# Performance work log

Measured on AMD Instinct MI355X. Metric: run time of the kernel, lower is better.

## Reference

```python
import jax, jax.numpy as jnp
import numpy as np

N_NODES = 100000


def _gcn_norm(edge_index, num_nodes):
    # PyG GCNConv default: add self-loops, symmetric normalization.
    src = jnp.concatenate([edge_index[0], jnp.arange(num_nodes, dtype=edge_index.dtype)])
    dst = jnp.concatenate([edge_index[1], jnp.arange(num_nodes, dtype=edge_index.dtype)])
    deg = jax.ops.segment_sum(jnp.ones_like(dst, dtype=jnp.float32), dst, num_segments=num_nodes)
    dis = jnp.where(deg > 0, jax.lax.rsqrt(deg), 0.0)  # deg^{-1/2}
    norm = dis[src] * dis[dst]  # [E + N]
    return src, dst, norm


def _gcn_conv(x, W, b, src, dst, norm, num_nodes):
    h = x @ W.T                      # [N, out] transform first (out < in)
    msg = h[src] * norm[:, None]     # gather + per-edge scale
    agg = jax.ops.segment_sum(msg, dst, num_segments=num_nodes)  # scatter-add
    return agg + b


def setup_inputs() -> dict:
    key = jax.random.key(0)
    ks = jax.random.split(key, 12)
    E = 3200000
    x = jax.random.normal(ks[0], (N_NODES, 128), dtype=jnp.float32)
    edge_index = jax.random.randint(ks[1], (2, E), 0, N_NODES, dtype=jnp.int64)
    s = lambda k, sh, fan: jax.random.normal(k, sh, dtype=jnp.float32) * (1.0 / np.sqrt(fan))
    return {
        "x": x,
        "edge_index": edge_index,
        "W1": s(ks[2], (32, 128), 128), "b1": jnp.zeros((32,), jnp.float32),
        "W2": s(ks[3], (16, 32), 32),   "b2": jnp.zeros((16,), jnp.float32),
        "w_ih": s(ks[4], (32, 16), 16), "w_hh": s(ks[5], (32, 8), 8),
        "b_ih": s(ks[6], (32,), 8),     "b_hh": s(ks[7], (32,), 8),
        "W_out": s(ks[8], (1, 8), 8),   "b_out": jnp.zeros((1,), jnp.float32),
    }


def reference(x, edge_index, W1, b1, W2, b2, w_ih, w_hh, b_ih, b_hh, W_out, b_out):
    src, dst, norm = _gcn_norm(edge_index, N_NODES)
    h = jax.nn.relu(_gcn_conv(x, W1, b1, src, dst, norm, N_NODES))   # [N, 32]
    h = jax.nn.relu(_gcn_conv(h, W2, b2, src, dst, norm, N_NODES))   # [N, 16]
    # Single-timestep LSTM with h0 = c0 = 0 (gate order: i, f, g, o).
    gates = h @ w_ih.T + b_ih + b_hh   # [N, 32]; h0 @ w_hh.T term is zero
    i, f, g, o = jnp.split(gates, 4, axis=-1)
    c = jax.nn.sigmoid(i) * jnp.tanh(g)
    hh = jax.nn.sigmoid(o) * jnp.tanh(c)  # [N, 8]
    out = hh @ W_out.T + b_out            # [N, 1]
    return out.squeeze(-1)                # [N]
```

## Files before the change

kernel.cpp:

```cpp
#include <hip/hip_runtime.h>
#include <hip/hip_fp16.h>
#include <math.h>

static constexpr int N = 100000;
static constexpr int SHIFT = 7;
static constexpr int BUCKN = 1 << SHIFT;
static constexpr int NBUCK = (N + BUCKN - 1) >> SHIFT;
static constexpr int CHUNK = 16384;
static constexpr int STRIDE = 5120;
static constexpr int COLCAP = NBUCK * STRIDE;

__global__ __launch_bounds__(1024) void k_init(int* __restrict__ gcur) {
    int b = threadIdx.x;
    if (b < NBUCK) gcur[b] = b * STRIDE;
}

__global__ __launch_bounds__(1024) void k_part(const int* __restrict__ src,
                                               const int* __restrict__ dst,
                                               int* __restrict__ gcur,
                                               int* __restrict__ col, int E) {
    __shared__ int hl[NBUCK];
    __shared__ int cur[NBUCK];
    const int t = threadIdx.x, b = blockIdx.x;
    if (t < NBUCK) hl[t] = 0;
    __syncthreads();
    const int e0 = b * CHUNK;
    const int m = min(CHUNK, E - e0);
    for (int i = t; i < m; i += 1024) atomicAdd(&hl[dst[e0 + i] >> SHIFT], 1);
    __syncthreads();
    if (t < NBUCK) cur[t] = atomicAdd(&gcur[t], hl[t]);
    __syncthreads();
    for (int i = t; i < m; i += 1024) {
        int d = dst[e0 + i];
        int pos = atomicAdd(&cur[d >> SHIFT], 1);
        pos = min(max(pos, 0), COLCAP - 1);
        col[pos] = (src[e0 + i] & 0x1FFFF) | ((d & (BUCKN - 1)) << 17);
    }
}

__global__ __launch_bounds__(1024) void k_sort(const int* __restrict__ gcur,
                                               int* __restrict__ col,
                                               int* __restrict__ deg,
                                               int* __restrict__ row_start) {
    __shared__ int es[STRIDE];
    __shared__ int cnt[BUCKN];
    __shared__ int cur[BUCKN];
    const int t = threadIdx.x, buck = blockIdx.x;
    const int s0 = buck * STRIDE;
    int n = gcur[buck] - s0;
    n = max(0, min(n, STRIDE));
    if (t < BUCKN) cnt[t] = 0;
    __syncthreads();
    for (int i = t; i < n; i += 1024) {
        int p = col[s0 + i];
        es[i] = p;
        atomicAdd(&cnt[(p >> 17) & (BUCKN - 1)], 1);
    }
    __syncthreads();
    if (t < BUCKN) cur[t] = cnt[t];
    __syncthreads();
    for (int off = 1; off < BUCKN; off <<= 1) {
        int v = (t < BUCKN && t >= off) ? cur[t - off] : 0;
        __syncthreads();
        if (t < BUCKN) cur[t] += v;
        __syncthreads();
    }
    if (t < BUCKN) {
        int excl = cur[t] - cnt[t];
        int node = buck * BUCKN + t;
        if (node < N) {
            deg[node] = cnt[t];
            row_start[node] = s0 + excl;
        }
        cur[t] = excl;
    }
    __syncthreads();
    for (int i = t; i < n; i += 1024) {
        int p = es[i];
        int pos = atomicAdd(&cur[(p >> 17) & (BUCKN - 1)], 1);
        pos = min(max(pos, 0), STRIDE - 1);
        col[s0 + pos] = p & 0x1FFFF;
    }
}

__global__ __launch_bounds__(256) void k_xw1(
        const float* __restrict__ x, const float* __restrict__ W1,
        const int* __restrict__ deg, __half* __restrict__ g1h) {
    __shared__ float4 wtv[32 * 33];
    __shared__ float4 xsv[1024];
    const int t = threadIdx.x;
    const float4* W1v = (const float4*)W1;
    for (int idx = t; idx < 1024; idx += 256) {
        int j = idx >> 5, kb = idx & 31;
        wtv[kb * 33 + j] = W1v[idx];
    }
    const float4* x4 = (const float4*)x + (size_t)blockIdx.x * 1024;
    for (int idx = t; idx < 1024; idx += 256) xsv[idx] = x4[idx];
    __syncthreads();

    const int j = t & 31, ng = t >> 5;
    float a0 = 0.f, a1 = 0.f, a2 = 0.f, a3 = 0.f;
#pragma unroll 4
    for (int kb = 0; kb < 32; ++kb) {
        float4 w = wtv[kb * 33 + j];
        float4 x0 = xsv[(4 * ng + 0) * 32 + kb];
        float4 x1 = xsv[(4 * ng + 1) * 32 + kb];
        float4 x2 = xsv[(4 * ng + 2) * 32 + kb];
        float4 x3 = xsv[(4 * ng + 3) * 32 + kb];
        a0 = fmaf(w.x, x0.x, fmaf(w.y, x0.y, fmaf(w.z, x0.z, fmaf(w.w, x0.w, a0))));
        a1 = fmaf(w.x, x1.x, fmaf(w.y, x1.y, fmaf(w.z, x1.z, fmaf(w.w, x1.w, a1))));
        a2 = fmaf(w.x, x2.x, fmaf(w.y, x2.y, fmaf(w.z, x2.z, fmaf(w.w, x2.w, a2))));
        a3 = fmaf(w.x, x3.x, fmaf(w.y, x3.y, fmaf(w.z, x3.z, fmaf(w.w, x3.w, a3))));
    }
    const int nb = blockIdx.x * 32 + 4 * ng;
    g1h[(nb + 0) * 32 + j] = __float2half(a0 * rsqrtf((float)(deg[nb + 0] + 1)));
    g1h[(nb + 1) * 32 + j] = __float2half(a1 * rsqrtf((float)(deg[nb + 1] + 1)));
    g1h[(nb + 2) * 32 + j] = __float2half(a2 * rsqrtf((float)(deg[nb + 2] + 1)));
    g1h[(nb + 3) * 32 + j] = __float2half(a3 * rsqrtf((float)(deg[nb + 3] + 1)));
}

__global__ __launch_bounds__(256) void k_gather1(
        const int* __restrict__ row_start, const int* __restrict__ deg,
        const int* __restrict__ col, const __half* __restrict__ g1h,
        const float* __restrict__ b1, const float* __restrict__ W2,
        __half* __restrict__ g2h) {
    __shared__ float h1s[64 * 33];
    __shared__ float w2t[32 * 17];
    const int t = threadIdx.x;
    for (int idx = t; idx < 512; idx += 256) {
        int j = idx >> 5, k = idx & 31;
        w2t[k * 17 + j] = W2[idx];
    }
    const int lane = t & 63, w = t >> 6;
    const int q = lane & 3;
    const int nloc = w * 16 + (lane >> 2);
    const int node = blockIdx.x * 64 + nloc;
    const int nc = node < N ? node : N - 1;
    const int rs = row_start[nc];
    const int ne = (node < N) ? deg[nc] : 0;
    const uint4* g1v = (const uint4*)g1h;

    float acc[8];
    {
        uint4 rv = g1v[nc * 4 + q];
        const __half2* hp = (const __half2*)&rv;
#pragma unroll
        for (int m2 = 0; m2 < 4; ++m2) {
            float2 f = __half22float2(hp[m2]);
            acc[2 * m2] = f.x;
            acc[2 * m2 + 1] = f.y;
        }
    }
    for (int base = 0; base < ne; base += 16) {
        int sv[4];
#pragma unroll
        for (int c = 0; c < 4; ++c)
            sv[c] = (base + 4 * c + q < ne) ? col[rs + base + 4 * c + q] : 0;
        int idx[16];
#pragma unroll
        for (int c = 0; c < 4; ++c)
#pragma unroll
            for (int u = 0; u < 4; ++u)
                idx[4 * c + u] = min(__shfl(sv[c], u, 4), N - 1);
        uint4 rv[16];
#pragma unroll
        for (int u = 0; u < 16; ++u) rv[u] = g1v[idx[u] * 4 + q];
#pragma unroll
        for (int u = 0; u < 16; ++u) {
            float wt = (base + u < ne) ? 1.f : 0.f;
            const __half2* hp = (const __half2*)&rv[u];
#pragma unroll
            for (int m2 = 0; m2 < 4; ++m2) {
                float2 f = __half22float2(hp[m2]);
                acc[2 * m2]     = fmaf(wt, f.x, acc[2 * m2]);
                acc[2 * m2 + 1] = fmaf(wt, f.y, acc[2 * m2 + 1]);
            }
        }
    }
    {
        const float dis = rsqrtf((float)(ne + 1));
#pragma unroll
        for (int u = 0; u < 8; ++u) {
            float v = (node < N) ? (acc[u] * dis + b1[q * 8 + u]) : 0.f;
            h1s[nloc * 33 + q * 8 + u] = v > 0.f ? v : 0.f;
        }
    }
    __syncthreads();
    const int n2 = t >> 2, jq = (t & 3) * 4;
    const int node2 = blockIdx.x * 64 + n2;
    if (node2 < N) {
        float a0 = 0.f, a1 = 0.f, a2 = 0.f, a3 = 0.f;
        const float* hr = h1s + n2 * 33;
#pragma unroll
        for (int k = 0; k < 32; ++k) {
            float h = hr[k];
            a0 = fmaf(h, w2t[k * 17 + jq + 0], a0);
            a1 = fmaf(h, w2t[k * 17 + jq + 1], a1);
            a2 = fmaf(h, w2t[k * 17 + jq + 2], a2);
            a3 = fmaf(h, w2t[k * 17 + jq + 3], a3);
        }
        const float dis2 = rsqrtf((float)(deg[node2] + 1));
        __half2* g2p = (__half2*)(g2h + node2 * 16 + jq);
        g2p[0] = __floats2half2_rn(a0 * dis2, a1 * dis2);
        g2p[1] = __floats2half2_rn(a2 * dis2, a3 * dis2);
    }
}

__global__ __launch_bounds__(256) void k_gather2(
        const int* __restrict__ row_start, const int* __restrict__ deg,
        const int* __restrict__ col, const __half* __restrict__ g2h,
        const float* __restrict__ b2, float* __restrict__ h2) {
    const int t = threadIdx.x;
    const int lane = t & 63, w = t >> 6;
    const int q = lane & 1;
    const int node = blockIdx.x * 128 + w * 32 + (lane >> 1);
    const int nc = node < N ? node : N - 1;
    const int rs = row_start[nc];
    const int ne = (node < N) ? deg[nc] : 0;
    const uint4* g2v = (const uint4*)g2h;

    float acc[8];
    {
        uint4 rv = g2v[nc * 2 + q];
        const __half2* hp = (const __half2*)&rv;
#pragma unroll
        for (int m2 = 0; m2 < 4; ++m2) {
            float2 f = __half22float2(hp[m2]);
            acc[2 * m2] = f.x;
            acc[2 * m2 + 1] = f.y;
        }
    }
    for (int base = 0; base < ne; base += 16) {
        int sv[8];
#pragma unroll
        for (int c = 0; c < 8; ++c)
            sv[c] = (base + 2 * c + q < ne) ? col[rs + base + 2 * c + q] : 0;
        int idx[16];
#pragma unroll
        for (int c = 0; c < 8; ++c) {
            idx[2 * c]     = min(__shfl(sv[c], 0, 2), N - 1);
            idx[2 * c + 1] = min(__shfl(sv[c], 1, 2), N - 1);
        }
        uint4 rv[16];
#pragma unroll
        for (int u = 0; u < 16; ++u) rv[u] = g2v[idx[u] * 2 + q];
#pragma unroll
        for (int u = 0; u < 16; ++u) {
            float wt = (base + u < ne) ? 1.f : 0.f;
            const __half2* hp = (const __half2*)&rv[u];
#pragma unroll
            for (int m2 = 0; m2 < 4; ++m2) {
                float2 f = __half22float2(hp[m2]);
                acc[2 * m2]     = fmaf(wt, f.x, acc[2 * m2]);
                acc[2 * m2 + 1] = fmaf(wt, f.y, acc[2 * m2 + 1]);
            }
        }
    }
    if (node < N) {
        const float dis = rsqrtf((float)(ne + 1));
        float4* h2v = (float4*)h2;
#pragma unroll
        for (int h = 0; h < 2; ++h) {
            float4 o;
            float v0 = acc[4 * h + 0] * dis + b2[q * 8 + 4 * h + 0];
            float v1 = acc[4 * h + 1] * dis + b2[q * 8 + 4 * h + 1];
            float v2 = acc[4 * h + 2] * dis + b2[q * 8 + 4 * h + 2];
            float v3 = acc[4 * h + 3] * dis + b2[q * 8 + 4 * h + 3];
            o.x = v0 > 0.f ? v0 : 0.f;
            o.y = v1 > 0.f ? v1 : 0.f;
            o.z = v2 > 0.f ? v2 : 0.f;
            o.w = v3 > 0.f ? v3 : 0.f;
            h2v[node * 4 + q * 2 + h] = o;
        }
    }
}

__global__ __launch_bounds__(256) void k_final(
        const float* __restrict__ h2g,
        const float* __restrict__ w_ih, const float* __restrict__ b_ih,
        const float* __restrict__ b_hh, const float* __restrict__ W_out,
        const float* __restrict__ b_out, float* __restrict__ out) {
    __shared__ float wih[512];
    __shared__ float bias[32];
    __shared__ float wout[8];
    __shared__ float bo;
    const int t = threadIdx.x;
    for (int idx = t; idx < 512; idx += 256) wih[idx] = w_ih[idx];
    if (t < 32) bias[t] = b_ih[t] + b_hh[t];
    if (t < 8)  wout[t] = W_out[t];
    if (t == 0) bo = b_out[0];
    __syncthreads();

    const int i = blockIdx.x * 256 + t;
    if (i >= N) return;
    float h2[16];
    const float4* a4 = (const float4*)(h2g + (size_t)i * 16);
#pragma unroll
    for (int q = 0; q < 4; ++q) {
        float4 v = a4[q];
        h2[q * 4 + 0] = v.x; h2[q * 4 + 1] = v.y;
        h2[q * 4 + 2] = v.z; h2[q * 4 + 3] = v.w;
    }
    float oacc = 0.f;
#pragma unroll
    for (int q = 0; q < 8; ++q) {
        float gi = bias[q], gg = bias[16 + q], go = bias[24 + q];
#pragma unroll
        for (int k = 0; k < 16; ++k) {
            gi = fmaf(h2[k], wih[q * 16 + k], gi);
            gg = fmaf(h2[k], wih[(16 + q) * 16 + k], gg);
            go = fmaf(h2[k], wih[(24 + q) * 16 + k], go);
        }
        float c  = (1.f / (1.f + expf(-gi))) * tanhf(gg);
        float hh = (1.f / (1.f + expf(-go))) * tanhf(c);
        oacc = fmaf(hh, wout[q], oacc);
    }
    out[i] = oacc + bo;
}

extern "C" void kernel_launch(void* const* d_in, const int* in_sizes, int n_in,
                              void* d_out, int out_size, void* d_ws, size_t ws_size,
                              hipStream_t stream) {
    const float* x     = (const float*)d_in[0];
    const int*   ei    = (const int*)d_in[1];
    const float* W1    = (const float*)d_in[2];
    const float* b1    = (const float*)d_in[3];
    const float* W2    = (const float*)d_in[4];
    const float* b2    = (const float*)d_in[5];
    const float* w_ih  = (const float*)d_in[6];
    const float* b_ih  = (const float*)d_in[8];
    const float* b_hh  = (const float*)d_in[9];
    const float* W_out = (const float*)d_in[10];
    const float* b_out = (const float*)d_in[11];
    float* out = (float*)d_out;

    const int E = in_sizes[1] / 2;
    const int* src = ei;
    const int* dst = ei + E;
    const int BP = (E + CHUNK - 1) / CHUNK;

    int* col       = (int*)d_ws;
    int* deg       = col + COLCAP;
    int* row_start = deg + N;
    int* gcur      = row_start + N;
    int* base2     = gcur + 784;
    __half* g1h    = (__half*)base2;
    __half* g2h    = (__half*)(base2 + (size_t)N * 16);
    float* h2      = (float*)(base2 + (size_t)N * 24);

    k_init   <<<1,               1024, 0, stream>>>(gcur);
    k_part   <<<BP,              1024, 0, stream>>>(src, dst, gcur, col, E);
    k_sort   <<<NBUCK,           1024, 0, stream>>>(gcur, col, deg, row_start);
    k_xw1    <<<N / 32,          256,  0, stream>>>(x, W1, deg, g1h);
    k_gather1<<<(N + 63) / 64,   256,  0, stream>>>(row_start, deg, col, g1h, b1, W2, g2h);
    k_gather2<<<(N + 127) / 128, 256,  0, stream>>>(row_start, deg, col, g2h, b2, h2);
    k_final  <<<(N + 255) / 256, 256,  0, stream>>>(h2, w_ih, b_ih, b_hh, W_out, b_out, out);
}
```

Measured before the change: 257.9 us.

## Replace global-atomic bucket partition with block-local sorted chunks and header-driven gather

The partition kernel now sorts each chunk by bucket in shared memory and writes it out contiguously with per-block bucket offsets in a header table, instead of scattering edges through global atomic cursors. The sort kernel then gathers its bucket's runs from every chunk using a prefix sum over the headers, and writes the CSR columns into a separate array. The goal is coalesced writes, no global atomics and no init kernel. In exchange, the sort kernel reads many short, serially-walked runs per bucket, one thread per source chunk with a per-element loop, which may be slow.

Measured after the change: 261.7 us. No clear change (+1.5%).

```diff
diff --git a/kernel.cpp b/kernel.cpp
--- a/kernel.cpp
+++ b/kernel.cpp
@@ -6,21 +6,21 @@
 static constexpr int SHIFT = 7;
 static constexpr int BUCKN = 1 << SHIFT;
 static constexpr int NBUCK = (N + BUCKN - 1) >> SHIFT;
-static constexpr int CHUNK = 16384;
+static constexpr int HDRS  = NBUCK + 1;
+static constexpr int CHUNK = 8192;
+static constexpr int BPMAX = 512;
 static constexpr int STRIDE = 5120;
 static constexpr int COLCAP = NBUCK * STRIDE;
-
-__global__ __launch_bounds__(1024) void k_init(int* __restrict__ gcur) {
-    int b = threadIdx.x;
-    if (b < NBUCK) gcur[b] = b * STRIDE;
-}
+static constexpr int ES_CAP = STRIDE;
 
 __global__ __launch_bounds__(1024) void k_part(const int* __restrict__ src,
                                                const int* __restrict__ dst,
-                                               int* __restrict__ gcur,
-                                               int* __restrict__ col, int E) {
+                                               int* __restrict__ col,
+                                               int* __restrict__ hdr, int E) {
+    __shared__ int stage[CHUNK];
     __shared__ int hl[NBUCK];
     __shared__ int cur[NBUCK];
+    __shared__ int s[1024];
     const int t = threadIdx.x, b = blockIdx.x;
     if (t < NBUCK) hl[t] = 0;
     __syncthreads();
@@ -28,41 +28,85 @@
     const int m = min(CHUNK, E - e0);
     for (int i = t; i < m; i += 1024) atomicAdd(&hl[dst[e0 + i] >> SHIFT], 1);
     __syncthreads();
-    if (t < NBUCK) cur[t] = atomicAdd(&gcur[t], hl[t]);
+    int v = (t < NBUCK) ? hl[t] : 0;
+    s[t] = v;
+    __syncthreads();
+    for (int off = 1; off < 1024; off <<= 1) {
+        int u = (t >= off) ? s[t - off] : 0;
+        __syncthreads();
+        s[t] += u;
+        __syncthreads();
+    }
+    if (t < NBUCK) {
+        int excl = s[t] - v;
+        cur[t] = excl;
+        hdr[b * HDRS + t] = excl;
+    }
+    if (t == 0) hdr[b * HDRS + NBUCK] = m;
     __syncthreads();
     for (int i = t; i < m; i += 1024) {
         int d = dst[e0 + i];
         int pos = atomicAdd(&cur[d >> SHIFT], 1);
-        pos = min(max(pos, 0), COLCAP - 1);
-        col[pos] = (src[e0 + i] & 0x1FFFF) | ((d & (BUCKN - 1)) << 17);
-    }
-}
-
-__global__ __launch_bounds__(1024) void k_sort(const int* __restrict__ gcur,
-                                               int* __restrict__ col,
+        pos = min(max(pos, 0), CHUNK - 1);
+        stage[pos] = (src[e0 + i] & 0x1FFFF) | ((d & (BUCKN - 1)) << 17);
+    }
+    __syncthreads();
+    for (int i = t; i < m; i += 1024) col[e0 + i] = stage[i];
+}
+
+__global__ __launch_bounds__(1024) void k_sort(const int* __restrict__ col,
+                                               const int* __restrict__ hdr,
+                                               int* __restrict__ col2,
                                                int* __restrict__ deg,
-                                               int* __restrict__ row_start) {
-    __shared__ int es[STRIDE];
+                                               int* __restrict__ row_start, int BP) {
+    __shared__ int es[ES_CAP];
+    __shared__ int rlen[BPMAX];
+    __shared__ int rst[BPMAX];
+    __shared__ int s[BPMAX];
     __shared__ int cnt[BUCKN];
     __shared__ int cur[BUCKN];
+    __shared__ int ntot;
     const int t = threadIdx.x, buck = blockIdx.x;
-    const int s0 = buck * STRIDE;
-    int n = gcur[buck] - s0;
-    n = max(0, min(n, STRIDE));
+    if (t < BPMAX) { rlen[t] = 0; rst[t] = 0; }
+    __syncthreads();
+    if (t < BP) {
+        int a = hdr[t * HDRS + buck];
+        int e = hdr[t * HDRS + buck + 1];
+        rst[t] = min(max(a, 0), CHUNK);
+        rlen[t] = min(max(e - a, 0), CHUNK);
+    }
+    __syncthreads();
+    int v = (t < BPMAX) ? rlen[t] : 0;
+    if (t < BPMAX) s[t] = v;
+    __syncthreads();
+    for (int off = 1; off < BPMAX; off <<= 1) {
+        int u = (t >= off && t < BPMAX) ? s[t - off] : 0;
+        __syncthreads();
+        if (t < BPMAX) s[t] += u;
+        __syncthreads();
+    }
+    if (t == BPMAX - 1) ntot = min(s[BPMAX - 1], ES_CAP);
+    __syncthreads();
+    const int n = ntot;
+    if (t < BP) {
+        const int off0 = s[t] - v;
+        const int base = t * CHUNK + rst[t];
+        for (int k = 0; k < rlen[t]; ++k) {
+            int p = off0 + k;
+            if (p < ES_CAP) es[p] = col[base + k];
+        }
+    }
+    __syncthreads();
     if (t < BUCKN) cnt[t] = 0;
     __syncthreads();
-    for (int i = t; i < n; i += 1024) {
-        int p = col[s0 + i];
-        es[i] = p;
-        atomicAdd(&cnt[(p >> 17) & (BUCKN - 1)], 1);
-    }
+    for (int i = t; i < n; i += 1024) atomicAdd(&cnt[(es[i] >> 17) & (BUCKN - 1)], 1);
     __syncthreads();
     if (t < BUCKN) cur[t] = cnt[t];
     __syncthreads();
     for (int off = 1; off < BUCKN; off <<= 1) {
-        int v = (t < BUCKN && t >= off) ? cur[t - off] : 0;
-        __syncthreads();
-        if (t < BUCKN) cur[t] += v;
+        int u = (t < BUCKN && t >= off) ? cur[t - off] : 0;
+        __syncthreads();
+        if (t < BUCKN) cur[t] += u;
         __syncthreads();
     }
     if (t < BUCKN) {
@@ -70,7 +114,7 @@
         int node = buck * BUCKN + t;
         if (node < N) {
             deg[node] = cnt[t];
-            row_start[node] = s0 + excl;
+            row_start[node] = buck * STRIDE + excl;
         }
         cur[t] = excl;
     }
@@ -79,7 +123,7 @@
         int p = es[i];
         int pos = atomicAdd(&cur[(p >> 17) & (BUCKN - 1)], 1);
         pos = min(max(pos, 0), STRIDE - 1);
-        col[s0 + pos] = p & 0x1FFFF;
+        col2[buck * STRIDE + pos] = p & 0x1FFFF;
     }
 }
 
@@ -121,7 +165,7 @@
 
 __global__ __launch_bounds__(256) void k_gather1(
         const int* __restrict__ row_start, const int* __restrict__ deg,
-        const int* __restrict__ col, const __half* __restrict__ g1h,
+        const int* __restrict__ col2, const __half* __restrict__ g1h,
         const float* __restrict__ b1, const float* __restrict__ W2,
         __half* __restrict__ g2h) {
     __shared__ float h1s[64 * 33];
@@ -155,7 +199,7 @@
         int sv[4];
 #pragma unroll
         for (int c = 0; c < 4; ++c)
-            sv[c] = (base + 4 * c + q < ne) ? col[rs + base + 4 * c + q] : 0;
+            sv[c] = (base + 4 * c + q < ne) ? col2[rs + base + 4 * c + q] : 0;
         int idx[16];
 #pragma unroll
         for (int c = 0; c < 4; ++c)
@@ -208,7 +252,7 @@
 
 __global__ __launch_bounds__(256) void k_gather2(
         const int* __restrict__ row_start, const int* __restrict__ deg,
-        const int* __restrict__ col, const __half* __restrict__ g2h,
+        const int* __restrict__ col2, const __half* __restrict__ g2h,
         const float* __restrict__ b2, float* __restrict__ h2) {
     const int t = threadIdx.x;
     const int lane = t & 63, w = t >> 6;
@@ -234,7 +278,7 @@
         int sv[8];
 #pragma unroll
         for (int c = 0; c < 8; ++c)
-            sv[c] = (base + 2 * c + q < ne) ? col[rs + base + 2 * c + q] : 0;
+            sv[c] = (base + 2 * c + q < ne) ? col2[rs + base + 2 * c + q] : 0;
         int idx[16];
 #pragma unroll
         for (int c = 0; c < 8; ++c) {
@@ -340,19 +384,19 @@
     const int BP = (E + CHUNK - 1) / CHUNK;
 
     int* col       = (int*)d_ws;
-    int* deg       = col + COLCAP;
+    int* hdr       = col + (size_t)BPMAX * CHUNK;
+    int* col2      = hdr + (size_t)BPMAX * HDRS;
+    int* deg       = col2 + COLCAP;
     int* row_start = deg + N;
-    int* gcur      = row_start + N;
-    int* base2     = gcur + 784;
+    int* base2     = row_start + N;
     __half* g1h    = (__half*)base2;
     __half* g2h    = (__half*)(base2 + (size_t)N * 16);
     float* h2      = (float*)(base2 + (size_t)N * 24);
 
-    k_init   <<<1,               1024, 0, stream>>>(gcur);
-    k_part   <<<BP,              1024, 0, stream>>>(src, dst, gcur, col, E);
-    k_sort   <<<NBUCK,           1024, 0, stream>>>(gcur, col, deg, row_start);
+    k_part   <<<BP,              1024, 0, stream>>>(src, dst, col, hdr, E);
+    k_sort   <<<NBUCK,           1024, 0, stream>>>(col, hdr, col2, deg, row_start, BP);
     k_xw1    <<<N / 32,          256,  0, stream>>>(x, W1, deg, g1h);
-    k_gather1<<<(N + 63) / 64,   256,  0, stream>>>(row_start, deg, col, g1h, b1, W2, g2h);
-    k_gather2<<<(N + 127) / 128, 256,  0, stream>>>(row_start, deg, col, g2h, b2, h2);
+    k_gather1<<<(N + 63) / 64,   256,  0, stream>>>(row_start, deg, col2, g1h, b1, W2, g2h);
+    k_gather2<<<(N + 127) / 128, 256,  0, stream>>>(row_start, deg, col2, g2h, b2, h2);
     k_final  <<<(N + 255) / 256, 256,  0, stream>>>(h2, w_ih, b_ih, b_hh, W_out, b_out, out);
 }
```
